# Kernel tuning notes

Measured on AMD Instinct MI355X. Metric: run time of the kernel, lower is better.

## Reference

```python
import jax, jax.numpy as jnp
import numpy as np

NUM_HEAD = 16
D = 1024
HEAD_DIM = D // NUM_HEAD
EPS = 1e-5


def setup_inputs() -> dict:
    key = jax.random.key(0)
    ks = jax.random.split(key, 7)
    B, S = 2, 2048
    s = 1.0 / np.sqrt(D)
    return {
        "x": jax.random.normal(ks[0], (B, S, D), dtype=jnp.float32),
        "wq": jax.random.uniform(ks[1], (D, D), jnp.float32, -s, s),
        "bq": jax.random.uniform(ks[2], (D,), jnp.float32, -s, s),
        "wk": jax.random.uniform(ks[3], (D, D), jnp.float32, -s, s),
        "bk": jax.random.uniform(ks[4], (D,), jnp.float32, -s, s),
        "wv": jax.random.uniform(ks[5], (D, D), jnp.float32, -s, s),
        "bv": jax.random.uniform(ks[6], (D,), jnp.float32, -s, s),
        "gamma": jnp.ones((D,), jnp.float32),
        "beta": jnp.zeros((D,), jnp.float32),
    }


def reference(x, wq, bq, wk, bk, wv, bv, gamma, beta):
    B, S, Dm = x.shape
    # Linear: x @ W^T + b (torch convention), then split heads -> [B, H, S, hd]
    def proj(w, b):
        y = jnp.einsum("bsd,ed->bse", x, w) + b
        return y.reshape(B, S, NUM_HEAD, HEAD_DIM).transpose(0, 2, 1, 3)

    q = proj(wq, bq)
    k = proj(wk, bk)
    v = proj(wv, bv)

    scores = jnp.einsum("bhqd,bhkd->bhqk", q, k) / np.sqrt(HEAD_DIM).astype(x.dtype)
    attn = jax.nn.softmax(scores, axis=-1)
    out = jnp.einsum("bhqk,bhkd->bhqd", attn, v)
    out = out.transpose(0, 2, 1, 3).reshape(B, S, Dm)

    out = out + x
    mu = jnp.mean(out, axis=-1, keepdims=True)
    var = jnp.var(out, axis=-1, keepdims=True)
    out = (out - mu) * jax.lax.rsqrt(var + EPS) * gamma + beta
    return out
```

## Files before the change

### kernel.cpp

```cpp
#include <hip/hip_runtime.h>

typedef unsigned short u16;
typedef unsigned int   u32;
typedef __bf16 bf16x8 __attribute__((ext_vector_type(8)));
typedef float  f32x4  __attribute__((ext_vector_type(4)));

#define D_MODEL 1024
#define SEQ     2048
#define NHEAD   16
#define HD      64
#define SOFTMAX_SCL 0.18033688011112042f

__device__ __forceinline__ u16 f2bf(float f) {
    u32 u;
    __builtin_memcpy(&u, &f, 4);
    u32 r = (u + 0x7fffu + ((u >> 16) & 1u)) >> 16;
    return (u16)r;
}
__device__ __forceinline__ float bf2f(u16 v) {
    u32 u = ((u32)v) << 16;
    float f;
    __builtin_memcpy(&f, &u, 4);
    return f;
}

__device__ __forceinline__ void async_copy16(const u16* g, u16* l) {
    __builtin_amdgcn_global_load_lds(
        (__attribute__((address_space(1))) void*)g,
        (__attribute__((address_space(3))) void*)l, 16, 0, 0);
}

__device__ __forceinline__ uint2 pack4(float a, float b, float c, float d) {
    uint2 r;
    r.x = (u32)f2bf(a) | ((u32)f2bf(b) << 16);
    r.y = (u32)f2bf(c) | ((u32)f2bf(d) << 16);
    return r;
}

#define NX4 ((2 * SEQ * D_MODEL) / 4)
#define NW4 ((D_MODEL * D_MODEL) / 4)
__global__ __launch_bounds__(256) void conv_all(
    const float* __restrict__ x,  const float* __restrict__ wq,
    const float* __restrict__ wk, const float* __restrict__ wv,
    u16* __restrict__ xb, u16* __restrict__ wqb,
    u16* __restrict__ wkb, u16* __restrict__ wvb)
{
    int i = blockIdx.x * 256 + threadIdx.x;
    const float* src; u16* dst; int off;
    if (i < NX4)            { src = x;  dst = xb;  off = i; }
    else if (i < NX4 + NW4) { src = wq; dst = wqb; off = i - NX4; }
    else if (i < NX4 + 2 * NW4) { src = wk; dst = wkb; off = i - NX4 - NW4; }
    else                    { src = wv; dst = wvb; off = i - NX4 - 2 * NW4; }
    float4 a = ((const float4*)src)[off];
    ushort4 o;
    o.x = f2bf(a.x); o.y = f2bf(a.y); o.z = f2bf(a.z); o.w = f2bf(a.w);
    ((ushort4*)dst)[off] = o;
}

__global__ __launch_bounds__(256) void qkv_gemm(
    const u16* __restrict__ xb,
    const u16* __restrict__ wqb, const float* __restrict__ bq,
    const u16* __restrict__ wkb, const float* __restrict__ bk,
    const u16* __restrict__ wvb, const float* __restrict__ bv,
    u16* __restrict__ qb, u16* __restrict__ kb, u16* __restrict__ vt)
{
    const int bid  = blockIdx.x;
    const int pair = bid % 24;
    const int by   = bid / 24;
    const int z    = pair >> 3;
    const int bx   = pair & 7;

    const u16* Ap; const u16* Bp;
    int m0, n0;
    if (z < 2) {
        Ap = (z == 1) ? wkb : wqb;  Bp = xb;
        m0 = bx * 128;
        n0 = by * 128;
    } else {
        Ap = xb;  Bp = wvb;
        m0 = by * 128;
        n0 = bx * 128;
    }

    __shared__ u16 As[128 * 64];
    __shared__ u16 Bs[128 * 64];

    const int tid  = threadIdx.x;
    const int wave = tid >> 6;
    const int lane = tid & 63;
    const int quad = lane >> 4;
    const int l16  = lane & 15;
    const int wm   = wave >> 1;
    const int wn   = wave & 1;
    const int swz  = l16 & 7;

    int rr[4], co[4];
#pragma unroll
    for (int t = 0; t < 4; ++t) {
        int ch = (wave * 4 + t) * 64 + lane;
        rr[t] = ch >> 3;
        co[t] = ((ch & 7) ^ (rr[t] & 7)) * 8;
    }

    f32x4 acc[4][4] = {};

    for (int kt = 0; kt < D_MODEL; kt += 64) {
        __syncthreads();
#pragma unroll
        for (int t = 0; t < 4; ++t) {
            int chbase = (wave * 4 + t) * 64;
            async_copy16(Ap + (size_t)(m0 + rr[t]) * D_MODEL + kt + co[t], As + chbase * 8);
            async_copy16(Bp + (size_t)(n0 + rr[t]) * D_MODEL + kt + co[t], Bs + chbase * 8);
        }
        __syncthreads();

#pragma unroll
        for (int kc = 0; kc < 2; ++kc) {
            bf16x8 af[4], bf_[4];
#pragma unroll
            for (int i = 0; i < 4; ++i)
                af[i] = *(const bf16x8*)&As[(wm * 64 + i * 16 + l16) * 64 + (((kc * 4 + quad) ^ swz) << 3)];
#pragma unroll
            for (int j = 0; j < 4; ++j)
                bf_[j] = *(const bf16x8*)&Bs[(wn * 64 + j * 16 + l16) * 64 + (((kc * 4 + quad) ^ swz) << 3)];
            __builtin_amdgcn_s_setprio(1);
#pragma unroll
            for (int i = 0; i < 4; ++i)
#pragma unroll
                for (int j = 0; j < 4; ++j)
                    acc[i][j] = __builtin_amdgcn_mfma_f32_16x16x32_bf16(af[i], bf_[j], acc[i][j], 0, 0, 0);
            __builtin_amdgcn_s_setprio(0);
        }
    }

    if (z < 2) {
        const int chunk_lo = (quad & 1) * 4;
        u16* out = (z == 1) ? kb : qb;
        const float* bi = (z == 1) ? bk : bq;
        const float scl = (z == 1) ? 1.0f : SOFTMAX_SCL;
        const int fblk = m0 + wm * 64;
#pragma unroll
        for (int i = 0; i < 4; ++i) {
            const int fb = fblk + i * 16 + quad * 4;
            float4 b4 = *(const float4*)&bi[fb];
            const int chunk = i * 2 + (quad >> 1);
#pragma unroll
            for (int j = 0; j < 4; ++j) {
                int token = n0 + wn * 64 + j * 16 + l16;
                uint2 pk = pack4((acc[i][j][0] + b4.x) * scl,
                                 (acc[i][j][1] + b4.y) * scl,
                                 (acc[i][j][2] + b4.z) * scl,
                                 (acc[i][j][3] + b4.w) * scl);
                size_t addr = (size_t)token * D_MODEL + fblk
                            + ((chunk ^ (token & 7)) << 3) + chunk_lo;
                *(uint2*)&out[addr] = pk;
            }
        }
    } else {
#pragma unroll
        for (int j = 0; j < 4; ++j) {
            int feat = n0 + wn * 64 + j * 16 + l16;
            float bias = bv[feat];
            int hh = feat >> 6, d = feat & 63;
            const size_t rowbase = ((size_t)hh * HD + d) * SEQ;
#pragma unroll
            for (int i = 0; i < 4; ++i) {
                int tok = m0 + wm * 64 + i * 16 + quad * 4;
                int b = tok >> 11, s = tok & 2047;
                const int nchunk = (i >> 1) * 4 + quad;
                const int nlo    = (i & 1) * 4;
                uint2 pk = pack4(acc[i][j][0] + bias, acc[i][j][1] + bias,
                                 acc[i][j][2] + bias, acc[i][j][3] + bias);
                size_t addr = (size_t)b * NHEAD * HD * SEQ + rowbase
                            + (s & ~63) + ((nchunk ^ (d & 7)) << 3) + nlo;
                *(uint2*)&vt[addr] = pk;
            }
        }
    }
}

__global__ __launch_bounds__(256) void attn_kernel(
    const u16* __restrict__ qb, const u16* __restrict__ kb, const u16* __restrict__ vtg,
    u16* __restrict__ abp, float* __restrict__ lsums)
{
    const int bid  = blockIdx.x;
    const int bh   = bid & 31;
    const int b    = bh >> 4;
    const int h    = bh & 15;
    const int q0   = ((bid >> 5) & 7) * 256;
    const int half = bid >> 8;

    const int tid  = threadIdx.x;
    const int wave = tid >> 6;
    const int lane = tid & 63;
    const int quad = lane >> 4;
    const int l16  = lane & 15;
    const int swz  = l16 & 7;

    __shared__ u16 Ks[2 * 4096];
    __shared__ u16 Vt[2 * 4096];

    const size_t kbase = (size_t)b * SEQ * D_MODEL + h * 64;
    const size_t vbase = (size_t)(b * NHEAD + h) * HD * SEQ;

    bf16x8 aq[4][2];
#pragma unroll
    for (int rb = 0; rb < 4; ++rb) {
        const int qrow = q0 + wave * 64 + rb * 16 + l16;
        const u16* qrp = qb + (size_t)qrow * D_MODEL + h * 64;
        aq[rb][0] = *(const bf16x8*)(qrp + ((quad ^ swz) << 3));
        aq[rb][1] = *(const bf16x8*)(qrp + (((4 + quad) ^ swz) << 3));
    }

    const int r0 = tid >> 3, r1 = (tid + 256) >> 3;
    const int cs8 = (tid & 7) * 8;
    const u16* kg0 = kb + kbase + (size_t)(half * 1024 + r0) * D_MODEL + cs8;
    const u16* kg1 = kb + kbase + (size_t)(half * 1024 + r1) * D_MODEL + cs8;
    const u16* vg0 = vtg + vbase + (size_t)r0 * SEQ + half * 1024 + cs8;
    const u16* vg1 = vtg + vbase + (size_t)r1 * SEQ + half * 1024 + cs8;
    const int wofs = wave * 512;

    f32x4 oacc[4][4] = {};
    float lsum[4] = {};

    async_copy16(kg0, Ks + wofs);
    async_copy16(kg1, Ks + 2048 + wofs);
    async_copy16(vg0, Vt + wofs);
    async_copy16(vg1, Vt + 2048 + wofs);
    kg0 += 64 * D_MODEL; kg1 += 64 * D_MODEL;
    vg0 += 64;           vg1 += 64;

    for (int t = 0; t < 16; ++t) {
        const int cur = (t & 1) << 12;
        const int nxt = cur ^ 4096;

        __builtin_amdgcn_s_barrier();
        if (t < 15) {
            async_copy16(kg0, Ks + nxt + wofs);
            async_copy16(kg1, Ks + nxt + 2048 + wofs);
            async_copy16(vg0, Vt + nxt + wofs);
            async_copy16(vg1, Vt + nxt + 2048 + wofs);
            kg0 += 64 * D_MODEL; kg1 += 64 * D_MODEL;
            vg0 += 64;           vg1 += 64;
            asm volatile("s_waitcnt vmcnt(4)" ::: "memory");
        } else {
            asm volatile("s_waitcnt vmcnt(0)" ::: "memory");
        }
        __builtin_amdgcn_s_barrier();

        const u16* Kc = Ks + cur;
        const u16* Vc = Vt + cur;

        f32x4 sacc[4][4] = {};
#pragma unroll
        for (int c = 0; c < 2; ++c) {
            bf16x8 bk_[4];
#pragma unroll
            for (int nb = 0; nb < 4; ++nb)
                bk_[nb] = *(const bf16x8*)&Kc[(nb * 16 + l16) * 64 + (((c * 4 + quad) ^ swz) << 3)];
            __builtin_amdgcn_s_setprio(1);
#pragma unroll
            for (int rb = 0; rb < 4; ++rb)
#pragma unroll
                for (int nb = 0; nb < 4; ++nb)
                    sacc[rb][nb] = __builtin_amdgcn_mfma_f32_16x16x32_bf16(bk_[nb], aq[rb][c], sacc[rb][nb], 0, 0, 0);
            __builtin_amdgcn_s_setprio(0);
        }

        bf16x8 ap[4][2];
#pragma unroll
        for (int rb = 0; rb < 4; ++rb) {
            u32 w[4][2];
#pragma unroll
            for (int nb = 0; nb < 4; ++nb) {
                float e0 = __builtin_amdgcn_exp2f(sacc[rb][nb][0]);
                float e1 = __builtin_amdgcn_exp2f(sacc[rb][nb][1]);
                float e2 = __builtin_amdgcn_exp2f(sacc[rb][nb][2]);
                float e3 = __builtin_amdgcn_exp2f(sacc[rb][nb][3]);
                lsum[rb] += (e0 + e1) + (e2 + e3);
                u32 b0, b1, b2, b3;
                __builtin_memcpy(&b0, &e0, 4); __builtin_memcpy(&b1, &e1, 4);
                __builtin_memcpy(&b2, &e2, 4); __builtin_memcpy(&b3, &e3, 4);
                w[nb][0] = __builtin_amdgcn_perm(b1, b0, 0x07060302);
                w[nb][1] = __builtin_amdgcn_perm(b3, b2, 0x07060302);
            }
            union { u32 d[4]; bf16x8 v; } u0, u1;
            u0.d[0] = w[0][0]; u0.d[1] = w[0][1]; u0.d[2] = w[1][0]; u0.d[3] = w[1][1];
            u1.d[0] = w[2][0]; u1.d[1] = w[2][1]; u1.d[2] = w[3][0]; u1.d[3] = w[3][1];
            ap[rb][0] = u0.v;
            ap[rb][1] = u1.v;
        }

#pragma unroll
        for (int c = 0; c < 2; ++c) {
            bf16x8 bv_[4];
#pragma unroll
            for (int nb = 0; nb < 4; ++nb)
                bv_[nb] = *(const bf16x8*)&Vc[(nb * 16 + l16) * 64 + (((c * 4 + quad) ^ swz) << 3)];
            __builtin_amdgcn_s_setprio(1);
#pragma unroll
            for (int rb = 0; rb < 4; ++rb)
#pragma unroll
                for (int nb = 0; nb < 4; ++nb)
                    oacc[rb][nb] = __builtin_amdgcn_mfma_f32_16x16x32_bf16(ap[rb][c], bv_[nb], oacc[rb][nb], 0, 0, 0);
            __builtin_amdgcn_s_setprio(0);
        }
    }

#pragma unroll
    for (int rb = 0; rb < 4; ++rb) {
        float s = lsum[rb];
        s += __shfl_xor(s, 16, 64);
        s += __shfl_xor(s, 32, 64);
        if (lane < 16)
            lsums[((size_t)bh * 2 + half) * SEQ + q0 + wave * 64 + rb * 16 + lane] = s;
#pragma unroll
        for (int r = 0; r < 4; ++r) {
            int row = q0 + wave * 64 + rb * 16 + quad * 4 + r;
#pragma unroll
            for (int nb = 0; nb < 4; ++nb) {
                int d = nb * 16 + l16;
                abp[(size_t)half * SEQ * 2 * D_MODEL
                    + ((size_t)b * SEQ + row) * D_MODEL + h * 64 + d] = f2bf(oacc[rb][nb][r]);
            }
        }
    }
}

__global__ __launch_bounds__(256) void add_ln(
    const u16* __restrict__ abp, const float* __restrict__ lsums,
    const float* __restrict__ x,
    const float* __restrict__ gamma, const float* __restrict__ beta,
    float* __restrict__ out)
{
    const int row = blockIdx.x;
    const int tid = threadIdx.x;
    const size_t rb = (size_t)row * D_MODEL;
    const int b = row >> 11, s = row & 2047;
    const int h = tid >> 4;
    const int bh = b * NHEAD + h;

    float l = lsums[(size_t)bh * 2 * SEQ + s] + lsums[((size_t)bh * 2 + 1) * SEQ + s];
    float inv = 1.0f / l;

    uint2 a0 = ((const uint2*)(abp + rb))[tid];
    uint2 a1 = ((const uint2*)(abp + (size_t)SEQ * 2 * D_MODEL + rb))[tid];
    float4 xb = ((const float4*)(x + rb))[tid];

    float v[4];
    v[0] = (bf2f((u16)(a0.x & 0xffff)) + bf2f((u16)(a1.x & 0xffff))) * inv + xb.x;
    v[1] = (bf2f((u16)(a0.x >> 16))    + bf2f((u16)(a1.x >> 16)))    * inv + xb.y;
    v[2] = (bf2f((u16)(a0.y & 0xffff)) + bf2f((u16)(a1.y & 0xffff))) * inv + xb.z;
    v[3] = (bf2f((u16)(a0.y >> 16))    + bf2f((u16)(a1.y >> 16)))    * inv + xb.w;

    float sm  = v[0] + v[1] + v[2] + v[3];
    float s2 = v[0]*v[0] + v[1]*v[1] + v[2]*v[2] + v[3]*v[3];
#pragma unroll
    for (int off = 1; off < 64; off <<= 1) {
        sm += __shfl_xor(sm, off, 64);
        s2 += __shfl_xor(s2, off, 64);
    }

    __shared__ float red[2][4];
    int wave = tid >> 6, lane = tid & 63;
    if (lane == 0) { red[0][wave] = sm; red[1][wave] = s2; }
    __syncthreads();
    float st  = red[0][0] + red[0][1] + red[0][2] + red[0][3];
    float s2t = red[1][0] + red[1][1] + red[1][2] + red[1][3];

    float mu   = st * (1.0f / D_MODEL);
    float var  = s2t * (1.0f / D_MODEL) - mu * mu;
    float rstd = rsqrtf(var + 1e-5f);

    float4 g  = ((const float4*)(gamma))[tid];
    float4 bt = ((const float4*)(beta))[tid];
    float4 o;
    o.x = (v[0] - mu) * rstd * g.x + bt.x;
    o.y = (v[1] - mu) * rstd * g.y + bt.y;
    o.z = (v[2] - mu) * rstd * g.z + bt.z;
    o.w = (v[3] - mu) * rstd * g.w + bt.w;
    ((float4*)(out + rb))[tid] = o;
}

extern "C" void kernel_launch(void* const* d_in, const int* in_sizes, int n_in,
                              void* d_out, int out_size, void* d_ws, size_t ws_size,
                              hipStream_t stream) {
    const float* x     = (const float*)d_in[0];
    const float* wq    = (const float*)d_in[1];
    const float* bq    = (const float*)d_in[2];
    const float* wk    = (const float*)d_in[3];
    const float* bk    = (const float*)d_in[4];
    const float* wv    = (const float*)d_in[5];
    const float* bv    = (const float*)d_in[6];
    const float* gamma = (const float*)d_in[7];
    const float* beta  = (const float*)d_in[8];
    float* outp = (float*)d_out;

    char* ws = (char*)d_ws;
    u16*   xb    = (u16*)(ws);
    u16*   wqb   = (u16*)(ws + ((size_t)8  << 20));
    u16*   wkb   = (u16*)(ws + ((size_t)10 << 20));
    u16*   wvb   = (u16*)(ws + ((size_t)12 << 20));
    u16*   qb    = (u16*)(ws + ((size_t)16 << 20));
    u16*   kb    = (u16*)(ws + ((size_t)24 << 20));
    u16*   vt    = (u16*)(ws + ((size_t)32 << 20));
    u16*   abp   = (u16*)(ws + ((size_t)40 << 20));
    float* lsums = (float*)(ws + ((size_t)56 << 20));

    conv_all<<<dim3((NX4 + 3 * NW4) / 256), 256, 0, stream>>>(
        x, wq, wk, wv, xb, wqb, wkb, wvb);
    qkv_gemm<<<dim3(24 * 32), 256, 0, stream>>>(xb, wqb, bq, wkb, bk, wvb, bv, qb, kb, vt);
    attn_kernel<<<dim3(512), 256, 0, stream>>>(qb, kb, vt, abp, lsums);
    add_ln<<<dim3(2 * SEQ), 256, 0, stream>>>(abp, lsums, x, gamma, beta, outp);
}
```

Before: 192.5 us.

## Shrink attention query tile to 64 rows per block, quadrupling grid size

Each attention block now processes 64 query rows (16 per wave) instead of 256 (64 per wave), and the grid grows from 512 to 2048 blocks. This cuts register pressure for the score and output accumulators and raises occupancy and CU load balance on a GPU with many CUs. In exchange, every K/V tile is loaded from global memory into shared memory four times as often, and each loaded tile feeds four times fewer MFMAs, lowering arithmetic intensity.

After: 186.2 us. -3.3%, faster.

```diff
diff --git a/kernel.cpp b/kernel.cpp
--- a/kernel.cpp
+++ b/kernel.cpp
@@ -187,8 +187,8 @@
     const int bh   = bid & 31;
     const int b    = bh >> 4;
     const int h    = bh & 15;
-    const int q0   = ((bid >> 5) & 7) * 256;
-    const int half = bid >> 8;
+    const int q0   = ((bid >> 5) & 31) * 64;
+    const int half = bid >> 10;
 
     const int tid  = threadIdx.x;
     const int wave = tid >> 6;
@@ -203,13 +203,12 @@
     const size_t kbase = (size_t)b * SEQ * D_MODEL + h * 64;
     const size_t vbase = (size_t)(b * NHEAD + h) * HD * SEQ;
 
-    bf16x8 aq[4][2];
-#pragma unroll
-    for (int rb = 0; rb < 4; ++rb) {
-        const int qrow = q0 + wave * 64 + rb * 16 + l16;
+    bf16x8 aq[2];
+    {
+        const int qrow = q0 + wave * 16 + l16;
         const u16* qrp = qb + (size_t)qrow * D_MODEL + h * 64;
-        aq[rb][0] = *(const bf16x8*)(qrp + ((quad ^ swz) << 3));
-        aq[rb][1] = *(const bf16x8*)(qrp + (((4 + quad) ^ swz) << 3));
+        aq[0] = *(const bf16x8*)(qrp + ((quad ^ swz) << 3));
+        aq[1] = *(const bf16x8*)(qrp + (((4 + quad) ^ swz) << 3));
     }
 
     const int r0 = tid >> 3, r1 = (tid + 256) >> 3;
@@ -220,8 +219,8 @@
     const u16* vg1 = vtg + vbase + (size_t)r1 * SEQ + half * 1024 + cs8;
     const int wofs = wave * 512;
 
-    f32x4 oacc[4][4] = {};
-    float lsum[4] = {};
+    f32x4 oacc[4] = {};
+    float lsum = 0.0f;
 
     async_copy16(kg0, Ks + wofs);
     async_copy16(kg1, Ks + 2048 + wofs);
@@ -251,7 +250,7 @@
         const u16* Kc = Ks + cur;
         const u16* Vc = Vt + cur;
 
-        f32x4 sacc[4][4] = {};
+        f32x4 sacc[4] = {};
 #pragma unroll
         for (int c = 0; c < 2; ++c) {
             bf16x8 bk_[4];
@@ -260,24 +259,21 @@
                 bk_[nb] = *(const bf16x8*)&Kc[(nb * 16 + l16) * 64 + (((c * 4 + quad) ^ swz) << 3)];
             __builtin_amdgcn_s_setprio(1);
 #pragma unroll
-            for (int rb = 0; rb < 4; ++rb)
-#pragma unroll
-                for (int nb = 0; nb < 4; ++nb)
-                    sacc[rb][nb] = __builtin_amdgcn_mfma_f32_16x16x32_bf16(bk_[nb], aq[rb][c], sacc[rb][nb], 0, 0, 0);
+            for (int nb = 0; nb < 4; ++nb)
+                sacc[nb] = __builtin_amdgcn_mfma_f32_16x16x32_bf16(bk_[nb], aq[c], sacc[nb], 0, 0, 0);
             __builtin_amdgcn_s_setprio(0);
         }
 
-        bf16x8 ap[4][2];
-#pragma unroll
-        for (int rb = 0; rb < 4; ++rb) {
+        bf16x8 ap[2];
+        {
             u32 w[4][2];
 #pragma unroll
             for (int nb = 0; nb < 4; ++nb) {
-                float e0 = __builtin_amdgcn_exp2f(sacc[rb][nb][0]);
-                float e1 = __builtin_amdgcn_exp2f(sacc[rb][nb][1]);
-                float e2 = __builtin_amdgcn_exp2f(sacc[rb][nb][2]);
-                float e3 = __builtin_amdgcn_exp2f(sacc[rb][nb][3]);
-                lsum[rb] += (e0 + e1) + (e2 + e3);
+                float e0 = __builtin_amdgcn_exp2f(sacc[nb][0]);
+                float e1 = __builtin_amdgcn_exp2f(sacc[nb][1]);
+                float e2 = __builtin_amdgcn_exp2f(sacc[nb][2]);
+                float e3 = __builtin_amdgcn_exp2f(sacc[nb][3]);
+                lsum += (e0 + e1) + (e2 + e3);
                 u32 b0, b1, b2, b3;
                 __builtin_memcpy(&b0, &e0, 4); __builtin_memcpy(&b1, &e1, 4);
                 __builtin_memcpy(&b2, &e2, 4); __builtin_memcpy(&b3, &e3, 4);
@@ -287,8 +283,8 @@
             union { u32 d[4]; bf16x8 v; } u0, u1;
             u0.d[0] = w[0][0]; u0.d[1] = w[0][1]; u0.d[2] = w[1][0]; u0.d[3] = w[1][1];
             u1.d[0] = w[2][0]; u1.d[1] = w[2][1]; u1.d[2] = w[3][0]; u1.d[3] = w[3][1];
-            ap[rb][0] = u0.v;
-            ap[rb][1] = u1.v;
+            ap[0] = u0.v;
+            ap[1] = u1.v;
         }
 
 #pragma unroll
@@ -299,29 +295,26 @@
                 bv_[nb] = *(const bf16x8*)&Vc[(nb * 16 + l16) * 64 + (((c * 4 + quad) ^ swz) << 3)];
             __builtin_amdgcn_s_setprio(1);
 #pragma unroll
-            for (int rb = 0; rb < 4; ++rb)
-#pragma unroll
-                for (int nb = 0; nb < 4; ++nb)
-                    oacc[rb][nb] = __builtin_amdgcn_mfma_f32_16x16x32_bf16(ap[rb][c], bv_[nb], oacc[rb][nb], 0, 0, 0);
+            for (int nb = 0; nb < 4; ++nb)
+                oacc[nb] = __builtin_amdgcn_mfma_f32_16x16x32_bf16(ap[c], bv_[nb], oacc[nb], 0, 0, 0);
             __builtin_amdgcn_s_setprio(0);
         }
     }
 
-#pragma unroll
-    for (int rb = 0; rb < 4; ++rb) {
-        float s = lsum[rb];
+    {
+        float s = lsum;
         s += __shfl_xor(s, 16, 64);
         s += __shfl_xor(s, 32, 64);
         if (lane < 16)
-            lsums[((size_t)bh * 2 + half) * SEQ + q0 + wave * 64 + rb * 16 + lane] = s;
+            lsums[((size_t)bh * 2 + half) * SEQ + q0 + wave * 16 + lane] = s;
 #pragma unroll
         for (int r = 0; r < 4; ++r) {
-            int row = q0 + wave * 64 + rb * 16 + quad * 4 + r;
+            int row = q0 + wave * 16 + quad * 4 + r;
 #pragma unroll
             for (int nb = 0; nb < 4; ++nb) {
                 int d = nb * 16 + l16;
                 abp[(size_t)half * SEQ * 2 * D_MODEL
-                    + ((size_t)b * SEQ + row) * D_MODEL + h * 64 + d] = f2bf(oacc[rb][nb][r]);
+                    + ((size_t)b * SEQ + row) * D_MODEL + h * 64 + d] = f2bf(oacc[nb][r]);
             }
         }
     }
@@ -410,6 +403,6 @@
     conv_all<<<dim3((NX4 + 3 * NW4) / 256), 256, 0, stream>>>(
         x, wq, wk, wv, xb, wqb, wkb, wvb);
     qkv_gemm<<<dim3(24 * 32), 256, 0, stream>>>(xb, wqb, bq, wkb, bk, wvb, bv, qb, kb, vt);
-    attn_kernel<<<dim3(512), 256, 0, stream>>>(qb, kb, vt, abp, lsums);
+    attn_kernel<<<dim3(2048), 256, 0, stream>>>(qb, kb, vt, abp, lsums);
     add_ln<<<dim3(2 * SEQ), 256, 0, stream>>>(abp, lsums, x, gamma, beta, outp);
 }
```
